# Kernel tuning notes

Measured on AMD Instinct MI355X. Metric: run time of the kernel, lower is better.

## Reference

```python
import jax, jax.numpy as jnp
import numpy as np

RH, RW = 40, 64          # render image height/width
SAM_HW = 64              # SAM ViT-H feature map spatial size
FEAT_DIM = 17            # voxel_feature_dim
GAUSSIAN_SEM_WEIGHT = 1.0


def nearest_resize(x, oh, ow):
    # torch F.interpolate mode='nearest': idx = floor(out_idx * in/out)
    ih, iw = x.shape[-2], x.shape[-1]
    ri = jnp.floor(jnp.arange(oh) * (ih / oh)).astype(jnp.int32)
    ci = jnp.floor(jnp.arange(ow) * (iw / ow)).astype(jnp.int32)
    return x[..., ri, :][..., ci]


def bilinear_resize(x, oh, ow):
    # torch bilinear, align_corners=False (half-pixel centers)
    ih, iw = x.shape[-2], x.shape[-1]
    def axis(isz, osz):
        src = (jnp.arange(osz, dtype=x.dtype) + 0.5) * (isz / osz) - 0.5
        i0 = jnp.clip(jnp.floor(src), 0, isz - 1).astype(jnp.int32)
        i1 = jnp.clip(i0 + 1, 0, isz - 1)
        w = jnp.clip(src - i0.astype(x.dtype), 0.0, 1.0)
        return i0, i1, w
    r0, r1, wr = axis(ih, oh)
    c0, c1, wc = axis(iw, ow)
    xr = x[..., r0, :] * (1 - wr)[:, None] + x[..., r1, :] * wr[:, None]
    return xr[..., c0] * (1 - wc) + xr[..., c1] * wc


def quat_to_rot(q):  # q: [N,4] normalized (w,x,y,z)
    w, x, y, z = q[:, 0], q[:, 1], q[:, 2], q[:, 3]
    R = jnp.stack([
        1 - 2 * (y * y + z * z), 2 * (x * y - w * z), 2 * (x * z + w * y),
        2 * (x * y + w * z), 1 - 2 * (x * x + z * z), 2 * (y * z - w * x),
        2 * (x * z - w * y), 2 * (y * z + w * x), 1 - 2 * (x * x + y * y)], -1)
    return R.reshape(-1, 3, 3)


def sam_proj(x, W1, b1, g1, be1, W2, b2, g2, be2, W3, b3):
    # Linear -> LayerNorm -> LeakyReLU (x2) -> Linear, all on last dim
    def ln(h, g, b):
        mu = h.mean(-1, keepdims=True)
        var = ((h - mu) ** 2).mean(-1, keepdims=True)
        return (h - mu) / jnp.sqrt(var + 1e-5) * g + b
    h = jax.nn.leaky_relu(ln(x @ W1.T + b1, g1, be1), 0.01)
    h = jax.nn.leaky_relu(ln(h @ W2.T + b2, g2, be2), 0.01)
    return h @ W3.T + b3


def render_feature_map(xyz, feats, opac, scal, quat, vm, intr):
    # Differentiable EWA Gaussian-splat feature rasterizer (3DGS-style math).
    N = xyz.shape[0]
    Rw, t = vm[:3, :3], vm[:3, 3]
    cam = xyz @ Rw.T + t                      # [N,3] camera coords
    x, y, z = cam[:, 0], cam[:, 1], cam[:, 2]
    fx, fy, cx, cy = intr[0], intr[1], intr[2], intr[3]
    zc = jnp.maximum(z, 1e-3)
    u = fx * x / zc + cx
    v = fy * y / zc + cy
    # 3D covariance Sigma = R S S^T R^T, transformed to camera then projected
    Rq = quat_to_rot(quat)
    M = Rq * scal[:, None, :]
    cov3 = M @ jnp.swapaxes(M, 1, 2)          # [N,3,3]
    covw = jnp.einsum('ij,njk,lk->nil', Rw, cov3, Rw)
    inv_z = 1.0 / zc
    zero = jnp.zeros_like(z)
    J = jnp.stack([
        jnp.stack([fx * inv_z, zero, -fx * x * inv_z ** 2], -1),
        jnp.stack([zero, fy * inv_z, -fy * y * inv_z ** 2], -1)], 1)  # [N,2,3]
    cov2 = jnp.einsum('nij,njk,nlk->nil', J, covw, J)
    a = cov2[:, 0, 0] + 0.3
    bq = cov2[:, 0, 1]
    cc = cov2[:, 1, 1] + 0.3
    det = a * cc - bq * bq
    A, Bc, Cc = cc / det, -bq / det, a / det   # conic (inverse 2D cov)
    xx, yy = jnp.meshgrid(jnp.arange(RW, dtype=xyz.dtype), jnp.arange(RH, dtype=xyz.dtype))
    px, py = xx.reshape(-1), yy.reshape(-1)    # [P]
    dx = u[:, None] - px[None, :]              # [N,P]
    dy = v[:, None] - py[None, :]
    power = -0.5 * (A[:, None] * dx * dx + Cc[:, None] * dy * dy) - Bc[:, None] * dx * dy
    alpha = jnp.minimum(0.99, opac * jnp.exp(jnp.minimum(power, 0.0)))
    alpha = alpha * (z > 0.2).astype(alpha.dtype)[:, None]
    # depth-sorted alpha compositing
    order = jnp.argsort(z)
    a_s = alpha[order]                         # [N,P]
    f_s = feats[order]                         # [N,C]
    T = jnp.concatenate([jnp.ones((1, a_s.shape[1]), a_s.dtype),
                         jnp.cumprod(1.0 - a_s, axis=0)[:-1]], axis=0)
    out = jnp.einsum('np,nc->cp', a_s * T, f_s)  # white_background=False -> bg 0
    return out.reshape(FEAT_DIM, RH, RW)


def _forward(voxel_feats, opacity, sam_embd, sam_features, sam_masks, viewmat,
             intrins, pc_xyz, scales, rots, W1, b1, g1, be1, W2, b2, g2, be2, W3, b3):
    B, C = viewmat.shape[0], viewmat.shape[1]
    scal = jnp.exp(scales)
    quat = rots / jnp.linalg.norm(rots, axis=-1, keepdims=True)
    proj = lambda x: sam_proj(x, W1, b1, g1, be1, W2, b2, g2, be2, W3, b3)
    loss_batch = 0.0
    for b in range(B):
        vf = voxel_feats[b].reshape(-1, FEAT_DIM)
        op = opacity[b].reshape(-1, 1)
        loss_c = 0.0
        for c in range(C):
            fmap = render_feature_map(pc_xyz, vf, op, scal, quat, viewmat[b, c], intrins[b, c])
            # use_sam: L1 between rendered map and projected SAM embedding
            se = nearest_resize(sam_embd[b, c], RH, RW)          # [256,RH,RW]
            sed = proj(se.transpose(1, 2, 0))                    # [RH,RW,17]
            loss_c = loss_c + jnp.abs(fmap.transpose(1, 2, 0) - sed).mean()
            # SAM mask contrastive loss
            sf = sam_features[b, c]                              # [256,64,64]
            ldf = proj(sf.reshape(256, -1).T).T.reshape(FEAT_DIM, SAM_HW, SAM_HW)
            masks = sam_masks[b, c]                              # [M,200,200]
            lsm = nearest_resize(masks, SAM_HW, SAM_HW)          # [M,64,64]
            proto = jnp.einsum('mhw,chw->mc', lsm, ldf)
            proto = proto / jnp.maximum(lsm.sum((1, 2)), 1e-6)[:, None]
            prob = jax.nn.sigmoid(jnp.einsum('mc,chw->mhw', proto, fmap))
            frm = bilinear_resize(masks, RH, RW)
            frm = jnp.where(frm <= 0.5, 0.0, frm)
            bce = frm * jnp.log(prob + 1e-8) + (1 - frm) * jnp.log(1 - prob + 1e-8)
            loss_c = loss_c - bce.mean()
        loss_batch = loss_batch + loss_c / C
    return loss_batch / B * GAUSSIAN_SEM_WEIGHT


def setup_inputs() -> dict:
    key = jax.random.key(0)
    ks = jax.random.split(key, 10)
    vs = 2.0
    gx1 = np.arange(-40.0, 40.0 + vs - 0.1, vs)
    gx = (gx1[:40] + gx1[1:41]) / 2
    gy = gx.copy()
    gz1 = np.arange(-2.4, 13.6 + vs - 0.1, vs)
    gz = (gz1[:8] + gz1[1:9]) / 2
    X, Y, Z = np.meshgrid(gx, gy, gz, indexing='ij')
    pc_xyz = np.stack([X, Y, Z], -1).reshape(-1, 3).astype(np.float32)
    N = pc_xyz.shape[0]  # 12800
    # regular grid: 3-NN mean squared dist = vs^2 -> scales = log(sqrt(vs^2))
    scales = np.full((N, 3), np.log(vs), np.float32)
    rots = np.zeros((N, 4), np.float32); rots[:, 0] = 1.0
    vm = np.zeros((1, 2, 4, 4), np.float32)
    vm[0, :, 0, 0] = vm[0, :, 1, 1] = vm[0, :, 2, 2] = vm[0, :, 3, 3] = 1.0
    vm[0, 0, :3, 3] = [0.0, 0.0, 60.0]
    vm[0, 1, :3, 3] = [2.0, -1.0, 62.0]
    intr = np.tile(np.array([32.0, 20.0, 32.0, 20.0], np.float32), (1, 2, 1))
    inp = {
        'voxel_feats': jax.random.normal(ks[0], (1, N, 17), jnp.float32) * 0.5,
        'opacity': jax.random.uniform(ks[1], (1, N, 1), jnp.float32) * 0.1,
        'sam_embd': jax.random.normal(ks[2], (1, 2, 256, 64, 64), jnp.float32),
        'sam_features': jax.random.normal(ks[3], (1, 2, 256, 64, 64), jnp.float32),
        'sam_masks': (jax.random.uniform(ks[4], (1, 2, 16, 200, 200)) < 0.3).astype(jnp.float32),
        'viewmat': jnp.asarray(vm), 'intrins': jnp.asarray(intr),
        'pc_xyz': jnp.asarray(pc_xyz), 'scales': jnp.asarray(scales), 'rots': jnp.asarray(rots),
        'W1': jax.random.normal(ks[5], (64, 256), jnp.float32) * 0.05,
        'b1': jnp.zeros((64,), jnp.float32),
        'g1': jnp.ones((64,), jnp.float32), 'be1': jnp.zeros((64,), jnp.float32),
        'W2': jax.random.normal(ks[6], (64, 64), jnp.float32) * 0.1,
        'b2': jnp.zeros((64,), jnp.float32),
        'g2': jnp.ones((64,), jnp.float32), 'be2': jnp.zeros((64,), jnp.float32),
        'W3': jax.random.normal(ks[7], (17, 64), jnp.float32) * 0.1,
        'b3': jnp.zeros((17,), jnp.float32),
    }
    return inp


def reference(voxel_feats, opacity, sam_embd, sam_features, sam_masks, viewmat,
              intrins, pc_xyz, scales, rots, W1, b1, g1, be1, W2, b2, g2, be2, W3, b3):
    return _forward(voxel_feats, opacity, sam_embd, sam_features, sam_masks, viewmat,
                    intrins, pc_xyz, scales, rots, W1, b1, g1, be1, W2, b2, g2, be2, W3, b3)
```

## Files before the change

### kernel.cpp

```cpp
#include <hip/hip_runtime.h>
#include <math.h>

#define NPTS   12800
#define P_PIX  2560
#define NC     128
#define CHUNK  100
#define NRG    10
#define RANK_CHUNK 400
#define RT     4
#define MLP_PITCH 264

typedef short short8 __attribute__((ext_vector_type(8)));
typedef float f32x4 __attribute__((ext_vector_type(4)));
typedef _Float16 h16x2 __attribute__((ext_vector_type(2)));

union F2H { float f; unsigned int u; h16x2 h; unsigned short s[2]; };

__device__ __forceinline__ unsigned int packbf_tr(float a, float b) {
    return __builtin_amdgcn_perm(__float_as_uint(b), __float_as_uint(a), 0x07060302u);
}
__device__ __forceinline__ unsigned short bf_tr(float a) {
    return (unsigned short)(__float_as_uint(a) >> 16);
}
__device__ __forceinline__ float pack2h(float a, float b) {
    union { float f; _Float16 h[2]; } c;
    c.h[0] = (_Float16)a; c.h[1] = (_Float16)b;
    return c.f;
}
__device__ __forceinline__ float2 unpk2h(float w) {
    union { float f; _Float16 h[2]; } c; c.f = w;
    return make_float2((float)c.h[0], (float)c.h[1]);
}

__global__ __launch_bounds__(256) void prep_kernel(
    const float* __restrict__ xyz, const float* __restrict__ scales,
    const float* __restrict__ rots, const float* __restrict__ opacity,
    const float* __restrict__ viewmat, const float* __restrict__ intrins,
    unsigned long long* __restrict__ keys,
    float* __restrict__ pu, float* __restrict__ pv, float* __restrict__ prad,
    float* __restrict__ phA, float* __restrict__ phC, float* __restrict__ pnB,
    float* __restrict__ pop, int* __restrict__ rnk, float* __restrict__ out, int N) {
    int cam = blockIdx.y;
    int i = blockIdx.x * 256 + threadIdx.x;
    if (i >= N) return;
    int idx = cam * N + i;
    rnk[idx] = 0;
    if (idx == 0) out[0] = 0.0f;
    const float* vm = viewmat + cam * 16;
    const float* it = intrins + cam * 4;
    float fx = it[0], fy = it[1], cx = it[2], cy = it[3];
    float R00 = vm[0], R01 = vm[1], R02 = vm[2], t0 = vm[3];
    float R10 = vm[4], R11 = vm[5], R12 = vm[6], t1 = vm[7];
    float R20 = vm[8], R21 = vm[9], R22 = vm[10], t2 = vm[11];
    float X = xyz[i * 3], Y = xyz[i * 3 + 1], Z = xyz[i * 3 + 2];
    float x = R00 * X + R01 * Y + R02 * Z + t0;
    float y = R10 * X + R11 * Y + R12 * Z + t1;
    float z = R20 * X + R21 * Y + R22 * Z + t2;
    float zc = fmaxf(z, 0.001f);
    float iz = 1.0f / zc;
    float u = fx * x * iz + cx;
    float v = fy * y * iz + cy;
    float qw = rots[i * 4], qx = rots[i * 4 + 1], qy = rots[i * 4 + 2], qz = rots[i * 4 + 3];
    float qn = 1.0f / sqrtf(qw * qw + qx * qx + qy * qy + qz * qz);
    qw *= qn; qx *= qn; qy *= qn; qz *= qn;
    float s0 = expf(scales[i * 3]), s1 = expf(scales[i * 3 + 1]), s2 = expf(scales[i * 3 + 2]);
    float Rq[3][3] = {
        {1 - 2 * (qy * qy + qz * qz), 2 * (qx * qy - qw * qz), 2 * (qx * qz + qw * qy)},
        {2 * (qx * qy + qw * qz), 1 - 2 * (qx * qx + qz * qz), 2 * (qy * qz - qw * qx)},
        {2 * (qx * qz - qw * qy), 2 * (qy * qz + qw * qx), 1 - 2 * (qx * qx + qy * qy)}};
    float M[3][3];
    #pragma unroll
    for (int r = 0; r < 3; ++r) { M[r][0] = Rq[r][0] * s0; M[r][1] = Rq[r][1] * s1; M[r][2] = Rq[r][2] * s2; }
    float c3[3][3];
    #pragma unroll
    for (int a = 0; a < 3; ++a)
        #pragma unroll
        for (int b = 0; b < 3; ++b)
            c3[a][b] = M[a][0] * M[b][0] + M[a][1] * M[b][1] + M[a][2] * M[b][2];
    float Rw[3][3] = {{R00, R01, R02}, {R10, R11, R12}, {R20, R21, R22}};
    float Wt[3][3];
    #pragma unroll
    for (int a = 0; a < 3; ++a)
        #pragma unroll
        for (int b = 0; b < 3; ++b)
            Wt[a][b] = Rw[a][0] * c3[0][b] + Rw[a][1] * c3[1][b] + Rw[a][2] * c3[2][b];
    float cw[3][3];
    #pragma unroll
    for (int a = 0; a < 3; ++a)
        #pragma unroll
        for (int b = 0; b < 3; ++b)
            cw[a][b] = Wt[a][0] * Rw[b][0] + Wt[a][1] * Rw[b][1] + Wt[a][2] * Rw[b][2];
    float j00 = fx * iz, j02 = -fx * x * iz * iz;
    float j11 = fy * iz, j12 = -fy * y * iz * iz;
    float c00 = j00 * j00 * cw[0][0] + 2.0f * j00 * j02 * cw[0][2] + j02 * j02 * cw[2][2];
    float c01 = j00 * j11 * cw[0][1] + j00 * j12 * cw[0][2] + j02 * j11 * cw[2][1] + j02 * j12 * cw[2][2];
    float c11 = j11 * j11 * cw[1][1] + 2.0f * j11 * j12 * cw[1][2] + j12 * j12 * cw[2][2];
    float a = c00 + 0.3f, bq = c01, cc = c11 + 0.3f;
    float det = a * cc - bq * bq;
    float A = cc / det, Bc = -bq / det, Cc = a / det;
    float lmin = 0.5f * ((A + Cc) - sqrtf((A - Cc) * (A - Cc) + 4.0f * Bc * Bc));
    lmin = fmaxf(lmin, 1e-20f);
    float opv = (z > 0.2f) ? opacity[i] : 0.0f;
    float rad = -1.0f;
    if (opv > 0.0f) {
        float tcut = logf(opv) + 18.42f;
        if (tcut > 0.0f) rad = sqrtf(2.0f * tcut / lmin);
    }
    pu[idx] = u; pv[idx] = v; prad[idx] = rad;
    phA[idx] = -0.5f * A; phC[idx] = -0.5f * Cc; pnB[idx] = -Bc;
    pop[idx] = opv;
    unsigned int zb = __float_as_uint(z);
    zb = (zb & 0x80000000u) ? ~zb : (zb | 0x80000000u);
    keys[idx] = ((unsigned long long)zb << 32) | (unsigned int)i;
}

__global__ __launch_bounds__(256) void rank_kernel(const unsigned long long* __restrict__ keys,
                                                   int* __restrict__ rnk, int N) {
    __shared__ unsigned long long sk[RANK_CHUNK];
    int cam = blockIdx.z;
    const unsigned long long* K = keys + (size_t)cam * N;
    int jbase = blockIdx.y * RANK_CHUNK;
    int jcnt = min(RANK_CHUNK, N - jbase);
    for (int t = threadIdx.x; t < jcnt; t += 256) sk[t] = K[jbase + t];
    __syncthreads();
    int i0 = blockIdx.x * (256 * RT) + threadIdx.x;
    unsigned long long ki[RT];
    int cnt[RT];
    #pragma unroll
    for (int t = 0; t < RT; ++t) {
        int i = i0 + t * 256;
        ki[t] = (i < N) ? K[i] : 0xFFFFFFFFFFFFFFFFull;
        cnt[t] = 0;
    }
    #pragma unroll 4
    for (int j = 0; j < jcnt; ++j) {
        unsigned long long kj = sk[j];
        #pragma unroll
        for (int t = 0; t < RT; ++t) cnt[t] += (kj < ki[t]) ? 1 : 0;
    }
    #pragma unroll
    for (int t = 0; t < RT; ++t) {
        int i = i0 + t * 256;
        if (i < N && cnt[t]) atomicAdd(rnk + (size_t)cam * N + i, cnt[t]);
    }
}

__global__ __launch_bounds__(256, 2) void scatter_mlp_kernel(
    const int* __restrict__ rnk,
    const float* __restrict__ pu, const float* __restrict__ pv, const float* __restrict__ prad,
    const float* __restrict__ phA, const float* __restrict__ phC, const float* __restrict__ pnB,
    const float* __restrict__ pop, const float* __restrict__ feats,
    float* __restrict__ rec, float2* __restrict__ vr,
    const float* __restrict__ embd, const float* __restrict__ sfeat,
    const float* __restrict__ W1, const float* __restrict__ b1,
    const float* __restrict__ g1, const float* __restrict__ be1,
    const float* __restrict__ W2, const float* __restrict__ b2,
    const float* __restrict__ g2, const float* __restrict__ be2,
    const float* __restrict__ W3, const float* __restrict__ b3,
    float* __restrict__ sed, float* __restrict__ ldf, int N) {
    __shared__ __align__(16) unsigned short smem[2 * 64 * MLP_PITCH];
    int bid = blockIdx.x;
    int tid = threadIdx.x;
    if (bid < 100) {
        int cam = bid / 50;
        int i = (bid % 50) * 256 + tid;
        if (i >= N) return;
        int idx = cam * N + i;
        int r = rnk[idx];
        float* d = rec + ((size_t)cam * N + r) * 16;
        d[0] = pu[idx]; d[1] = pv[idx];
        d[2] = pack2h(phA[idx], phC[idx]);
        d[3] = pack2h(pnB[idx], pop[idx]);
        const float* f = feats + (size_t)i * 17;
        #pragma unroll
        for (int j = 0; j < 8; ++j) d[4 + j] = pack2h(f[2 * j], f[2 * j + 1]);
        d[12] = pack2h(f[16], 0.0f);
        d[13] = 0.0f; d[14] = 0.0f; d[15] = 0.0f;
        vr[(size_t)cam * N + r] = make_float2(pv[idx], prad[idx]);
        return;
    }
    unsigned short* sX = smem;
    unsigned short* sW = smem + 64 * MLP_PITCH;
    unsigned int* sX32 = (unsigned int*)sX;
    unsigned int* sW32 = (unsigned int*)sW;
    int lane = tid & 63, wv = tid >> 6;
    int m = lane & 15, kq = lane >> 4, q4 = kq * 4;
    int tile = bid - 100;
    const float* xbase;
    if (tile < 80) {
        int cam = tile / 40; int r = tile - cam * 40;
        int ri = (r * 8) / 5;
        xbase = embd + (size_t)cam * 256 * 4096 + ri * 64;
    } else {
        int tt = tile - 80; int cam = tt >> 6;
        xbase = sfeat + (size_t)cam * 256 * 4096 + (tt & 63) * 64;
    }
    const float4* xf4 = (const float4*)xbase;
    for (int idx = tid; idx < 2048; idx += 256) {
        int kp = idx >> 4, q = idx & 15;
        float4 xv0 = xf4[(size_t)(2 * kp) * 1024 + q];
        float4 xv1 = xf4[(size_t)(2 * kp + 1) * 1024 + q];
        int r = q * 4;
        sX32[(r + 0) * 132 + kp] = packbf_tr(xv0.x, xv1.x);
        sX32[(r + 1) * 132 + kp] = packbf_tr(xv0.y, xv1.y);
        sX32[(r + 2) * 132 + kp] = packbf_tr(xv0.z, xv1.z);
        sX32[(r + 3) * 132 + kp] = packbf_tr(xv0.w, xv1.w);
    }
    const float2* wf2 = (const float2*)W1;
    for (int idx = tid; idx < 8192; idx += 256) {
        int n = idx >> 7, k2 = idx & 127;
        float2 wp = wf2[n * 128 + k2];
        sW32[n * 132 + k2] = packbf_tr(wp.x, wp.y);
    }
    float b1v[4], g1v[4], be1v[4], b2v[4], g2v[4], be2v[4];
    #pragma unroll
    for (int nt = 0; nt < 4; ++nt) {
        int c = nt * 16 + m;
        b1v[nt] = b1[c]; g1v[nt] = g1[c]; be1v[nt] = be1[c];
        b2v[nt] = b2[c]; g2v[nt] = g2[c]; be2v[nt] = be2[c];
    }
    __syncthreads();
    f32x4 acc[4];
    #pragma unroll
    for (int nt = 0; nt < 4; ++nt) acc[nt] = (f32x4){0.f, 0.f, 0.f, 0.f};
    const unsigned short* aptr = sX + (wv * 16 + m) * MLP_PITCH + kq * 8;
    const unsigned short* bptr = sW + m * MLP_PITCH + kq * 8;
    #pragma unroll
    for (int ks = 0; ks < 8; ++ks) {
        short8 af = *(const short8*)(aptr + ks * 32);
        #pragma unroll
        for (int nt = 0; nt < 4; ++nt) {
            short8 bf = *(const short8*)(bptr + nt * 16 * MLP_PITCH + ks * 32);
            acc[nt] = __builtin_amdgcn_mfma_f32_16x16x32_bf16(af, bf, acc[nt], 0, 0, 0);
        }
    }
    __syncthreads();
    unsigned short* hbuf  = smem + wv * 16 * 72;
    unsigned short* hbuf2 = smem + (4 + wv) * 16 * 72;
    unsigned short* W2b = sW;
    unsigned short* W3b = sW + 64 * 72;
    unsigned int* W2b32 = (unsigned int*)W2b;
    unsigned int* W3b32 = (unsigned int*)W3b;
    const float2* w2f2 = (const float2*)W2;
    for (int i = tid; i < 2048; i += 256) {
        int n = i >> 5, k2 = i & 31;
        float2 wp = w2f2[n * 32 + k2];
        W2b32[n * 36 + k2] = packbf_tr(wp.x, wp.y);
    }
    const float2* w3f2 = (const float2*)W3;
    for (int i = tid; i < 1024; i += 256) {
        int n = i >> 5, k2 = i & 31;
        unsigned int v = 0;
        if (n < 17) { float2 wp = w3f2[n * 32 + k2]; v = packbf_tr(wp.x, wp.y); }
        W3b32[n * 36 + k2] = v;
    }
    #pragma unroll
    for (int rg = 0; rg < 4; ++rg) {
        float h0 = acc[0][rg] + b1v[0], h1 = acc[1][rg] + b1v[1];
        float h2 = acc[2][rg] + b1v[2], h3 = acc[3][rg] + b1v[3];
        float s = (h0 + h1) + (h2 + h3);
        s += __shfl_xor(s, 1); s += __shfl_xor(s, 2);
        s += __shfl_xor(s, 4); s += __shfl_xor(s, 8);
        float mu = s * (1.0f / 64.0f);
        float d0 = h0 - mu, d1 = h1 - mu, d2 = h2 - mu, d3 = h3 - mu;
        float vs = (d0 * d0 + d1 * d1) + (d2 * d2 + d3 * d3);
        vs += __shfl_xor(vs, 1); vs += __shfl_xor(vs, 2);
        vs += __shfl_xor(vs, 4); vs += __shfl_xor(vs, 8);
        float rstd = 1.0f / sqrtf(vs * (1.0f / 64.0f) + 1e-5f);
        float hn0 = d0 * rstd * g1v[0] + be1v[0]; hn0 = fmaxf(hn0, 0.01f * hn0);
        float hn1 = d1 * rstd * g1v[1] + be1v[1]; hn1 = fmaxf(hn1, 0.01f * hn1);
        float hn2 = d2 * rstd * g1v[2] + be1v[2]; hn2 = fmaxf(hn2, 0.01f * hn2);
        float hn3 = d3 * rstd * g1v[3] + be1v[3]; hn3 = fmaxf(hn3, 0.01f * hn3);
        int rr = (q4 + rg) * 72 + m;
        hbuf[rr] = bf_tr(hn0); hbuf[rr + 16] = bf_tr(hn1);
        hbuf[rr + 32] = bf_tr(hn2); hbuf[rr + 48] = bf_tr(hn3);
    }
    __syncthreads();
    f32x4 acc2[4];
    #pragma unroll
    for (int nt = 0; nt < 4; ++nt) acc2[nt] = (f32x4){0.f, 0.f, 0.f, 0.f};
    const unsigned short* a2p = hbuf + m * 72 + kq * 8;
    #pragma unroll
    for (int ks = 0; ks < 2; ++ks) {
        short8 af = *(const short8*)(a2p + ks * 32);
        #pragma unroll
        for (int nt = 0; nt < 4; ++nt) {
            short8 bf = *(const short8*)(W2b + (nt * 16 + m) * 72 + kq * 8 + ks * 32);
            acc2[nt] = __builtin_amdgcn_mfma_f32_16x16x32_bf16(af, bf, acc2[nt], 0, 0, 0);
        }
    }
    #pragma unroll
    for (int rg = 0; rg < 4; ++rg) {
        float h0 = acc2[0][rg] + b2v[0], h1 = acc2[1][rg] + b2v[1];
        float h2 = acc2[2][rg] + b2v[2], h3 = acc2[3][rg] + b2v[3];
        float s = (h0 + h1) + (h2 + h3);
        s += __shfl_xor(s, 1); s += __shfl_xor(s, 2);
        s += __shfl_xor(s, 4); s += __shfl_xor(s, 8);
        float mu = s * (1.0f / 64.0f);
        float d0 = h0 - mu, d1 = h1 - mu, d2 = h2 - mu, d3 = h3 - mu;
        float vs = (d0 * d0 + d1 * d1) + (d2 * d2 + d3 * d3);
        vs += __shfl_xor(vs, 1); vs += __shfl_xor(vs, 2);
        vs += __shfl_xor(vs, 4); vs += __shfl_xor(vs, 8);
        float rstd = 1.0f / sqrtf(vs * (1.0f / 64.0f) + 1e-5f);
        float hn0 = d0 * rstd * g2v[0] + be2v[0]; hn0 = fmaxf(hn0, 0.01f * hn0);
        float hn1 = d1 * rstd * g2v[1] + be2v[1]; hn1 = fmaxf(hn1, 0.01f * hn1);
        float hn2 = d2 * rstd * g2v[2] + be2v[2]; hn2 = fmaxf(hn2, 0.01f * hn2);
        float hn3 = d3 * rstd * g2v[3] + be2v[3]; hn3 = fmaxf(hn3, 0.01f * hn3);
        int rr = (q4 + rg) * 72 + m;
        hbuf2[rr] = bf_tr(hn0); hbuf2[rr + 16] = bf_tr(hn1);
        hbuf2[rr + 32] = bf_tr(hn2); hbuf2[rr + 48] = bf_tr(hn3);
    }
    f32x4 acc3[2];
    acc3[0] = (f32x4){0.f, 0.f, 0.f, 0.f};
    acc3[1] = (f32x4){0.f, 0.f, 0.f, 0.f};
    const unsigned short* a3p = hbuf2 + m * 72 + kq * 8;
    #pragma unroll
    for (int ks = 0; ks < 2; ++ks) {
        short8 af = *(const short8*)(a3p + ks * 32);
        #pragma unroll
        for (int nt = 0; nt < 2; ++nt) {
            short8 bf = *(const short8*)(W3b + (nt * 16 + m) * 72 + kq * 8 + ks * 32);
            acc3[nt] = __builtin_amdgcn_mfma_f32_16x16x32_bf16(af, bf, acc3[nt], 0, 0, 0);
        }
    }
    #pragma unroll
    for (int nt = 0; nt < 2; ++nt) {
        int c = nt * 16 + m;
        if (c < 17) {
            float b3v = b3[c];
            #pragma unroll
            for (int rg = 0; rg < 4; ++rg) {
                int row = tile * 64 + wv * 16 + q4 + rg;
                float val = acc3[nt][rg] + b3v;
                if (row < 5120) {
                    int cam = row / 2560; int p = row - cam * 2560;
                    sed[((size_t)cam * 2560 + p) * 17 + c] = val;
                } else {
                    int rr = row - 5120; int cam = rr >> 12; int t = rr & 4095;
                    ldf[((size_t)cam * 17 + c) * 4096 + t] = val;
                }
            }
        }
    }
}

__global__ __launch_bounds__(64) void splat_kernel(const float* __restrict__ rec,
                                                   const float2* __restrict__ vr,
                                                   float* __restrict__ partT,
                                                   unsigned int* __restrict__ partS32,
                                                   const float* __restrict__ masks,
                                                   const float* __restrict__ ldf,
                                                   float* __restrict__ proto, int N) {
    __shared__ __align__(16) float4 sRaw[CHUNK * 4];
    __shared__ __align__(16) float4 sCmp[CHUNK * 4];
    __shared__ unsigned char sIdx[CHUNK];
    int rg = blockIdx.x, ch = blockIdx.y, cam = blockIdx.z;
    int lane = threadIdx.x;
    if (rg == NRG) {
        int m = ch;
        if (m >= 16) return;
        const float* M = masks + ((size_t)cam * 16 + m) * 40000;
        float acc[18];
        #pragma unroll
        for (int j = 0; j < 18; ++j) acc[j] = 0.0f;
        for (int t = lane; t < 4096; t += 64) {
            int h = t >> 6, w = t & 63;
            int rh = (h * 25) >> 3, rw = (w * 25) >> 3;
            float lv = M[rh * 200 + rw];
            if (lv != 0.0f) {
                acc[17] += lv;
                const float* L = ldf + (size_t)cam * 17 * 4096 + t;
                #pragma unroll
                for (int c = 0; c < 17; ++c) acc[c] = fmaf(lv, L[(size_t)c * 4096], acc[c]);
            }
        }
        #pragma unroll
        for (int j = 0; j < 18; ++j) {
            float v = acc[j];
            #pragma unroll
            for (int o = 32; o; o >>= 1) v += __shfl_xor(v, o);
            acc[j] = v;
        }
        if (lane < 17)
            proto[((size_t)cam * 16 + m) * 17 + lane] = acc[lane] / fmaxf(acc[17], 1e-6f);
        return;
    }
    const float4* src = (const float4*)(rec + ((size_t)cam * N + ch * CHUNK) * 16);
    for (int t = lane; t < CHUNK * 4; t += 64) sRaw[t] = src[t];
    const float2* V = vr + (size_t)cam * N + ch * CHUNK;
    float cy = (float)(rg * 4) + 1.5f;
    int cnt = 0;
    for (int g = 0; g < CHUNK; g += 64) {
        int n = g + lane;
        bool pass = false;
        if (n < CHUNK) {
            float2 t = V[n];
            pass = fabsf(t.x - cy) <= t.y + 1.51f;
        }
        unsigned long long mask = __ballot(pass);
        int pre = __popcll(mask & ((1ull << lane) - 1ull));
        if (pass) sIdx[cnt + pre] = (unsigned char)n;
        cnt += __popcll(mask);
    }
    __syncthreads();
    for (int l = lane; l < cnt; l += 64) {
        int n = sIdx[l];
        sCmp[l * 4 + 0] = sRaw[n * 4 + 0];
        sCmp[l * 4 + 1] = sRaw[n * 4 + 1];
        sCmp[l * 4 + 2] = sRaw[n * 4 + 2];
        sCmp[l * 4 + 3] = sRaw[n * 4 + 3];
    }
    __syncthreads();
    int r0 = rg * 4;
    float px = (float)lane, py0 = (float)r0;
    float T0 = 1.0f, T1 = 1.0f, T2 = 1.0f, T3 = 1.0f;
    h16x2 acc[4][9];
    #pragma unroll
    for (int r = 0; r < 4; ++r)
        #pragma unroll
        for (int j = 0; j < 9; ++j) acc[r][j] = (h16x2){(_Float16)0.f, (_Float16)0.f};
    const float* sRf = (const float*)sCmp;
    for (int i = 0; i < cnt; ++i) {
        const float4* rp = sCmp + i * 4;
        float4 q0 = rp[0];
        float2 g0 = unpk2h(q0.z);
        float2 g1 = unpk2h(q0.w);
        float dx = q0.x - px;
        float dy = q0.y - py0;
        float ta = (g0.x * dx) * dx;
        float tb = g1.x * dx;
        float h2 = g0.y + g0.y;
        float p0 = fmaf(dy, fmaf(g0.y, dy, tb), ta);
        float e = fmaf(-h2, dy, g0.y - tb);
        float p1 = p0 + e; e += h2;
        float p2 = p1 + e; e += h2;
        float p3 = p2 + e;
        float a0 = fminf(0.99f, g1.y * __expf(fminf(p0, 0.0f)));
        float a1 = fminf(0.99f, g1.y * __expf(fminf(p1, 0.0f)));
        float a2 = fminf(0.99f, g1.y * __expf(fminf(p2, 0.0f)));
        float a3 = fminf(0.99f, g1.y * __expf(fminf(p3, 0.0f)));
        float w0 = a0 * T0, w1 = a1 * T1, w2 = a2 * T2, w3 = a3 * T3;
        T0 = fmaf(-T0, a0, T0); T1 = fmaf(-T1, a1, T1);
        T2 = fmaf(-T2, a2, T2); T3 = fmaf(-T3, a3, T3);
        h16x2 wh[4];
        wh[0] = (h16x2){(_Float16)w0, (_Float16)w0};
        wh[1] = (h16x2){(_Float16)w1, (_Float16)w1};
        wh[2] = (h16x2){(_Float16)w2, (_Float16)w2};
        wh[3] = (h16x2){(_Float16)w3, (_Float16)w3};
        float4 q1 = rp[1], q2 = rp[2];
        float fg = sRf[i * 16 + 12];
        F2H f[9];
        f[0].f = q1.x; f[1].f = q1.y; f[2].f = q1.z; f[3].f = q1.w;
        f[4].f = q2.x; f[5].f = q2.y; f[6].f = q2.z; f[7].f = q2.w;
        f[8].f = fg;
        #pragma unroll
        for (int r = 0; r < 4; ++r)
            #pragma unroll
            for (int j = 0; j < 9; ++j)
                acc[r][j] += wh[r] * f[j].h;
    }
    size_t cbase = (size_t)(cam * NC + ch);
    size_t p0i = (size_t)r0 * 64 + lane;
    partT[cbase * P_PIX + p0i]       = T0;
    partT[cbase * P_PIX + p0i + 64]  = T1;
    partT[cbase * P_PIX + p0i + 128] = T2;
    partT[cbase * P_PIX + p0i + 192] = T3;
    #pragma unroll
    for (int r = 0; r < 4; ++r) {
        #pragma unroll
        for (int cp = 0; cp < 9; ++cp) {
            F2H v; v.h = acc[r][cp];
            partS32[(cbase * 9 + cp) * P_PIX + p0i + (size_t)r * 64] = v.u;
        }
    }
}

__global__ __launch_bounds__(256) void combine_kernel(const float* __restrict__ partT,
                                                      const unsigned int* __restrict__ partS32,
                                                      float* __restrict__ fmap) {
    int idx = blockIdx.x * 256 + threadIdx.x;
    int p = idx % P_PIX;
    int rem = idx / P_PIX;
    int cp = rem % 9;
    int cam = rem / 9;
    float acc0 = 0.0f, acc1 = 0.0f, Tp = 1.0f;
    #pragma unroll 8
    for (int k = 0; k < NC; ++k) {
        size_t cb = (size_t)(cam * NC + k);
        float Tk = partT[cb * P_PIX + p];
        F2H v; v.u = partS32[(cb * 9 + cp) * P_PIX + p];
        acc0 = fmaf(Tp, (float)v.h[0], acc0);
        acc1 = fmaf(Tp, (float)v.h[1], acc1);
        Tp *= Tk;
    }
    int c = 2 * cp;
    fmap[((size_t)cam * 17 + c) * P_PIX + p] = acc0;
    if (c + 1 < 17) fmap[((size_t)cam * 17 + c + 1) * P_PIX + p] = acc1;
}

__device__ __forceinline__ void block_atomic_add(float v, float* target) {
    #pragma unroll
    for (int o = 32; o; o >>= 1) v += __shfl_xor(v, o);
    __shared__ float sred[4];
    int lane = threadIdx.x & 63, wv = threadIdx.x >> 6;
    if (lane == 0) sred[wv] = v;
    __syncthreads();
    if (threadIdx.x == 0) atomicAdd(target, sred[0] + sred[1] + sred[2] + sred[3]);
}

__global__ __launch_bounds__(256) void bce_kernel(const float* __restrict__ masks,
                                                  const float* __restrict__ proto,
                                                  const float* __restrict__ fmap,
                                                  const float* __restrict__ sed,
                                                  float* __restrict__ out) {
    int idx = blockIdx.x * 256 + threadIdx.x;
    int p = idx % P_PIX;
    int rem = idx / P_PIX;
    int m = rem & 15, cam = rem >> 4;
    const float* pr = proto + ((size_t)cam * 16 + m) * 17;
    float f[17];
    #pragma unroll
    for (int c = 0; c < 17; ++c) f[c] = fmap[((size_t)cam * 17 + c) * P_PIX + p];
    float sdot = 0;
    #pragma unroll
    for (int c = 0; c < 17; ++c) sdot = fmaf(pr[c], f[c], sdot);
    float prob = 1.0f / (1.0f + __expf(-sdot));
    int px = p & 63, py = p >> 6;
    float src_r = (py + 0.5f) * 5.0f - 0.5f;
    float src_c = (px + 0.5f) * 3.125f - 0.5f;
    int r0 = (int)fminf(fmaxf(floorf(src_r), 0.0f), 199.0f);
    int r1 = min(r0 + 1, 199);
    float wr = fminf(fmaxf(src_r - (float)r0, 0.0f), 1.0f);
    int c0 = (int)fminf(fmaxf(floorf(src_c), 0.0f), 199.0f);
    int c1 = min(c0 + 1, 199);
    float wc = fminf(fmaxf(src_c - (float)c0, 0.0f), 1.0f);
    const float* M = masks + ((size_t)cam * 16 + m) * 40000;
    float v00 = M[r0 * 200 + c0], v01 = M[r0 * 200 + c1];
    float v10 = M[r1 * 200 + c0], v11 = M[r1 * 200 + c1];
    float xr0 = v00 * (1.0f - wr) + v10 * wr;
    float xr1 = v01 * (1.0f - wr) + v11 * wr;
    float frm = xr0 * (1.0f - wc) + xr1 * wc;
    frm = (frm <= 0.5f) ? 0.0f : frm;
    float bce = frm * __logf(prob + 1e-8f) + (1.0f - frm) * __logf(1.0f - prob + 1e-8f);
    float val = bce * (-1.0f / (16.0f * 2560.0f * 2.0f));
    if (m == 0) {
        float ssum = 0.0f;
        const float* sp = sed + ((size_t)cam * P_PIX + p) * 17;
        #pragma unroll
        for (int c = 0; c < 17; ++c) ssum += fabsf(f[c] - sp[c]);
        val += ssum * (1.0f / (43520.0f * 2.0f));
    }
    block_atomic_add(val, out);
}

extern "C" void kernel_launch(void* const* d_in, const int* in_sizes, int n_in,
                              void* d_out, int out_size, void* d_ws, size_t ws_size,
                              hipStream_t stream) {
    const float* voxel_feats = (const float*)d_in[0];
    const float* opacity     = (const float*)d_in[1];
    const float* sam_embd    = (const float*)d_in[2];
    const float* sam_features= (const float*)d_in[3];
    const float* sam_masks   = (const float*)d_in[4];
    const float* viewmat     = (const float*)d_in[5];
    const float* intrins     = (const float*)d_in[6];
    const float* pc_xyz      = (const float*)d_in[7];
    const float* scales      = (const float*)d_in[8];
    const float* rots        = (const float*)d_in[9];
    const float* W1 = (const float*)d_in[10], *b1 = (const float*)d_in[11];
    const float* g1 = (const float*)d_in[12], *be1 = (const float*)d_in[13];
    const float* W2 = (const float*)d_in[14], *b2 = (const float*)d_in[15];
    const float* g2 = (const float*)d_in[16], *be2 = (const float*)d_in[17];
    const float* W3 = (const float*)d_in[18], *b3 = (const float*)d_in[19];
    float* out = (float*)d_out;
    const int N = in_sizes[7] / 3;

    char* w = (char*)d_ws;
    size_t off = 0;
    auto alloc = [&](size_t bytes) -> void* {
        off = (off + 255) & ~(size_t)255;
        void* p = w + off; off += bytes; return p;
    };
    int* rnk  = (int*)alloc((size_t)2 * N * sizeof(int));
    unsigned long long* keys = (unsigned long long*)alloc((size_t)2 * N * 8);
    float* params = (float*)alloc((size_t)7 * 2 * N * 4);
    float* pu  = params,           *pv  = params + 2 * N,  *prad = params + 4 * N;
    float* phA = params + 6 * N,   *phC = params + 8 * N,  *pnB  = params + 10 * N;
    float* pop = params + 12 * N;
    float* rec   = (float*)alloc((size_t)2 * N * 16 * 4);
    float2* vr   = (float2*)alloc((size_t)2 * N * 8);
    float* partT = (float*)alloc((size_t)2 * NC * P_PIX * 4);
    unsigned int* partS32 = (unsigned int*)alloc((size_t)2 * NC * 9 * P_PIX * 4);
    float* fmap  = (float*)alloc((size_t)2 * 17 * P_PIX * 4);
    float* sed   = (float*)alloc((size_t)2 * P_PIX * 17 * 4);
    float* ldf   = (float*)alloc((size_t)2 * 17 * 4096 * 4);
    float* proto = (float*)alloc((size_t)2 * 16 * 17 * 4);

    dim3 gprep((N + 255) / 256, 2);
    prep_kernel<<<gprep, 256, 0, stream>>>(pc_xyz, scales, rots, opacity, viewmat, intrins,
                                           keys, pu, pv, prad, phA, phC, pnB, pop, rnk, out, N);
    dim3 grank((N + 256 * RT - 1) / (256 * RT), (N + RANK_CHUNK - 1) / RANK_CHUNK, 2);
    rank_kernel<<<grank, 256, 0, stream>>>(keys, rnk, N);
    scatter_mlp_kernel<<<308, 256, 0, stream>>>(rnk, pu, pv, prad, phA, phC, pnB, pop,
                                                voxel_feats, rec, vr,
                                                sam_embd, sam_features, W1, b1, g1, be1,
                                                W2, b2, g2, be2, W3, b3, sed, ldf, N);
    dim3 gsplat(NRG + 1, NC, 2);
    splat_kernel<<<gsplat, 64, 0, stream>>>(rec, vr, partT, partS32,
                                            sam_masks, ldf, proto, N);
    combine_kernel<<<(2 * 9 * P_PIX) / 256, 256, 0, stream>>>(partT, partS32, fmap);
    bce_kernel<<<(2 * 16 * P_PIX) / 256, 256, 0, stream>>>(sam_masks, proto, fmap, sed, out);
}
```

Before: 227.9 us.

## Move prototype pooling into combine kernel and split combine per channel

Mask-prototype pooling moves out of the splat grid's extra row of 64-thread blocks and into the combine kernel, running as extra 256-thread blocks with a shared-memory cross-wave reduction. The partial-feature buffer changes from packed half pairs (9 words per pixel) to 17 separate half planes, so combine runs one thread per channel instead of per channel pair. This raises combine parallelism from 180 to 340 blocks and removes the proto blocks from the splat grid. The cost is twice as many partT loads in combine and narrower 16-bit scattered stores in splat.

```diff
diff --git a/kernel.cpp b/kernel.cpp
--- a/kernel.cpp
+++ b/kernel.cpp
@@ -347,44 +347,12 @@
 __global__ __launch_bounds__(64) void splat_kernel(const float* __restrict__ rec,
                                                    const float2* __restrict__ vr,
                                                    float* __restrict__ partT,
-                                                   unsigned int* __restrict__ partS32,
-                                                   const float* __restrict__ masks,
-                                                   const float* __restrict__ ldf,
-                                                   float* __restrict__ proto, int N) {
+                                                   unsigned short* __restrict__ partS, int N) {
     __shared__ __align__(16) float4 sRaw[CHUNK * 4];
     __shared__ __align__(16) float4 sCmp[CHUNK * 4];
     __shared__ unsigned char sIdx[CHUNK];
     int rg = blockIdx.x, ch = blockIdx.y, cam = blockIdx.z;
     int lane = threadIdx.x;
-    if (rg == NRG) {
-        int m = ch;
-        if (m >= 16) return;
-        const float* M = masks + ((size_t)cam * 16 + m) * 40000;
-        float acc[18];
-        #pragma unroll
-        for (int j = 0; j < 18; ++j) acc[j] = 0.0f;
-        for (int t = lane; t < 4096; t += 64) {
-            int h = t >> 6, w = t & 63;
-            int rh = (h * 25) >> 3, rw = (w * 25) >> 3;
-            float lv = M[rh * 200 + rw];
-            if (lv != 0.0f) {
-                acc[17] += lv;
-                const float* L = ldf + (size_t)cam * 17 * 4096 + t;
-                #pragma unroll
-                for (int c = 0; c < 17; ++c) acc[c] = fmaf(lv, L[(size_t)c * 4096], acc[c]);
-            }
-        }
-        #pragma unroll
-        for (int j = 0; j < 18; ++j) {
-            float v = acc[j];
-            #pragma unroll
-            for (int o = 32; o; o >>= 1) v += __shfl_xor(v, o);
-            acc[j] = v;
-        }
-        if (lane < 17)
-            proto[((size_t)cam * 16 + m) * 17 + lane] = acc[lane] / fmaxf(acc[17], 1e-6f);
-        return;
-    }
     const float4* src = (const float4*)(rec + ((size_t)cam * N + ch * CHUNK) * 16);
     for (int t = lane; t < CHUNK * 4; t += 64) sRaw[t] = src[t];
     const float2* V = vr + (size_t)cam * N + ch * CHUNK;
@@ -468,34 +436,71 @@
     #pragma unroll
     for (int r = 0; r < 4; ++r) {
         #pragma unroll
-        for (int cp = 0; cp < 9; ++cp) {
-            F2H v; v.h = acc[r][cp];
-            partS32[(cbase * 9 + cp) * P_PIX + p0i + (size_t)r * 64] = v.u;
-        }
-    }
-}
-
-__global__ __launch_bounds__(256) void combine_kernel(const float* __restrict__ partT,
-                                                      const unsigned int* __restrict__ partS32,
-                                                      float* __restrict__ fmap) {
-    int idx = blockIdx.x * 256 + threadIdx.x;
-    int p = idx % P_PIX;
-    int rem = idx / P_PIX;
-    int cp = rem % 9;
-    int cam = rem / 9;
-    float acc0 = 0.0f, acc1 = 0.0f, Tp = 1.0f;
-    #pragma unroll 8
-    for (int k = 0; k < NC; ++k) {
-        size_t cb = (size_t)(cam * NC + k);
-        float Tk = partT[cb * P_PIX + p];
-        F2H v; v.u = partS32[(cb * 9 + cp) * P_PIX + p];
-        acc0 = fmaf(Tp, (float)v.h[0], acc0);
-        acc1 = fmaf(Tp, (float)v.h[1], acc1);
-        Tp *= Tk;
-    }
-    int c = 2 * cp;
-    fmap[((size_t)cam * 17 + c) * P_PIX + p] = acc0;
-    if (c + 1 < 17) fmap[((size_t)cam * 17 + c + 1) * P_PIX + p] = acc1;
+        for (int c = 0; c < 17; ++c) {
+            F2H v; v.h = acc[r][c >> 1];
+            partS[(cbase * 17 + c) * P_PIX + p0i + (size_t)r * 64] = v.s[c & 1];
+        }
+    }
+}
+
+__global__ __launch_bounds__(256) void combine_proto_kernel(const float* __restrict__ partT,
+                                                            const unsigned short* __restrict__ partS,
+                                                            const float* __restrict__ masks,
+                                                            const float* __restrict__ ldf,
+                                                            float* __restrict__ fmap,
+                                                            float* __restrict__ proto) {
+    __shared__ float red[4][18];
+    int bid = blockIdx.x;
+    if (bid < 340) {
+        int idx = bid * 256 + threadIdx.x;
+        int p = idx % P_PIX;
+        int rem = idx / P_PIX;
+        int c = rem % 17;
+        int cam = rem / 17;
+        const _Float16* pS = (const _Float16*)partS;
+        float acc = 0.0f, Tp = 1.0f;
+        #pragma unroll 8
+        for (int k = 0; k < NC; ++k) {
+            size_t cb = (size_t)(cam * NC + k);
+            float Tk = partT[cb * P_PIX + p];
+            float S = (float)pS[(cb * 17 + c) * P_PIX + p];
+            acc = fmaf(Tp, S, acc);
+            Tp *= Tk;
+        }
+        fmap[((size_t)cam * 17 + c) * P_PIX + p] = acc;
+        return;
+    }
+    int t0 = bid - 340;
+    int m = t0 & 15, cam = t0 >> 4;
+    const float* M = masks + ((size_t)cam * 16 + m) * 40000;
+    float acc[18];
+    #pragma unroll
+    for (int j = 0; j < 18; ++j) acc[j] = 0.0f;
+    for (int t = threadIdx.x; t < 4096; t += 256) {
+        int h = t >> 6, w = t & 63;
+        int rh = (h * 25) >> 3, rw = (w * 25) >> 3;
+        float lv = M[rh * 200 + rw];
+        if (lv != 0.0f) {
+            acc[17] += lv;
+            const float* L = ldf + (size_t)cam * 17 * 4096 + t;
+            #pragma unroll
+            for (int c = 0; c < 17; ++c) acc[c] = fmaf(lv, L[(size_t)c * 4096], acc[c]);
+        }
+    }
+    int lane = threadIdx.x & 63, wv = threadIdx.x >> 6;
+    #pragma unroll
+    for (int j = 0; j < 18; ++j) {
+        float v = acc[j];
+        #pragma unroll
+        for (int o = 32; o; o >>= 1) v += __shfl_xor(v, o);
+        if (lane == 0) red[wv][j] = v;
+    }
+    __syncthreads();
+    if (threadIdx.x < 17) {
+        float sacc = red[0][threadIdx.x] + red[1][threadIdx.x] + red[2][threadIdx.x] + red[3][threadIdx.x];
+        float ms = red[0][17] + red[1][17] + red[2][17] + red[3][17];
+        proto[((size_t)cam * 16 + m) * 17 + threadIdx.x] = sacc / fmaxf(ms, 1e-6f);
+    }
 }
 
 __device__ __forceinline__ void block_atomic_add(float v, float* target) {
@@ -589,7 +594,7 @@
     float* rec   = (float*)alloc((size_t)2 * N * 16 * 4);
     float2* vr   = (float2*)alloc((size_t)2 * N * 8);
     float* partT = (float*)alloc((size_t)2 * NC * P_PIX * 4);
-    unsigned int* partS32 = (unsigned int*)alloc((size_t)2 * NC * 9 * P_PIX * 4);
+    unsigned short* partS = (unsigned short*)alloc((size_t)2 * NC * 17 * P_PIX * 2);
     float* fmap  = (float*)alloc((size_t)2 * 17 * P_PIX * 4);
     float* sed   = (float*)alloc((size_t)2 * P_PIX * 17 * 4);
     float* ldf   = (float*)alloc((size_t)2 * 17 * 4096 * 4);
@@ -604,9 +609,8 @@
                                                 voxel_feats, rec, vr,
                                                 sam_embd, sam_features, W1, b1, g1, be1,
                                                 W2, b2, g2, be2, W3, b3, sed, ldf, N);
-    dim3 gsplat(NRG + 1, NC, 2);
-    splat_kernel<<<gsplat, 64, 0, stream>>>(rec, vr, partT, partS32,
-                                            sam_masks, ldf, proto, N);
-    combine_kernel<<<(2 * 9 * P_PIX) / 256, 256, 0, stream>>>(partT, partS32, fmap);
+    dim3 gsplat(NRG, NC, 2);
+    splat_kernel<<<gsplat, 64, 0, stream>>>(rec, vr, partT, partS, N);
+    combine_proto_kernel<<<372, 256, 0, stream>>>(partT, partS, sam_masks, ldf, fmap, proto);
     bce_kernel<<<(2 * 16 * P_PIX) / 256, 256, 0, stream>>>(sam_masks, proto, fmap, sed, out);
 }
```

Result: faster. 214.2 us (-6.0%).
